# Kernel tuning notes

Hardware: AMD Instinct MI355X
Metric: run time of the kernel (lower is better)

Reference implementation:

```python
import jax, jax.numpy as jnp
import numpy as np

# Scalars from init_kwargs (qat_training=False inference path)
IN_ZP = 0
OUT_ZP = 0
IN_SCALE = 0.02
OUT_SCALE = 0.05
STRIDE = (1, 1)
PAD = (1, 1)      # (ph, pw); module pads (pw, pw, ph, ph) via F.pad
DIL = (1, 1)
GROUPS = 1
QMIN, QMAX = -128, 127  # get_quantized_range(8)


def setup_inputs() -> dict:
    key = jax.random.key(0)
    k1, k2, k3, k4 = jax.random.split(key, 4)
    x = jax.random.randint(k1, (32, 128, 56, 56), -128, 128, dtype=jnp.int32).astype(jnp.int8)
    weight = jax.random.randint(k2, (256, 128, 3, 3), -128, 128, dtype=jnp.int32).astype(jnp.int8)
    bias = jax.random.randint(k3, (256,), -1000, 1000, dtype=jnp.int32)
    weight_scale = jax.random.uniform(k4, (256,), minval=1e-3, maxval=1e-2, dtype=jnp.float32)
    return {"x": x, "weight": weight, "bias": bias, "weight_scale": weight_scale}


def reference(x, weight, bias, weight_scale):
    # Pad spatial dims with the input zero point (matches F.pad(..., value=input_zero_point))
    xp = jnp.pad(x.astype(jnp.int32),
                 ((0, 0), (0, 0), (PAD[0], PAD[0]), (PAD[1], PAD[1])),
                 constant_values=IN_ZP)
    # Exact int32-accumulate convolution (torch CPU path)
    acc = jax.lax.conv_general_dilated(
        xp, weight.astype(jnp.int32),
        window_strides=STRIDE, padding='VALID', rhs_dilation=DIL,
        dimension_numbers=('NCHW', 'OIHW', 'NCHW'),
        feature_group_count=GROUPS, preferred_element_type=jnp.int32)
    acc = acc + bias[None, :, None, None]
    # Per-output-channel requantization
    scale = (IN_SCALE * weight_scale / OUT_SCALE)[None, :, None, None]
    out = acc.astype(jnp.float32) * scale + OUT_ZP
    out = jnp.clip(jnp.round(out), QMIN, QMAX).astype(jnp.int8)
    return out
```

## Files before the change

kernel.cpp:

```cpp
#include <hip/hip_runtime.h>
#include <hip/hip_bf16.h>
#include <stdint.h>


#define NB   32
#define CIN  128
#define HO   56
#define WO   56
#define KOUT 256
#define HP   58
#define ROWB (HP * CIN)

typedef int v4i  __attribute__((ext_vector_type(4)));
typedef int v16i __attribute__((ext_vector_type(16)));

static __device__ __forceinline__ void gload_lds16(const int8_t* g, int8_t* l) {
  __builtin_amdgcn_global_load_lds(
      (const __attribute__((address_space(1))) void*)g,
      (__attribute__((address_space(3))) void*)l, 16, 0, 0);
}

__global__ __launch_bounds__(256) void pack_x_kernel(const int* __restrict__ x,
                                                     int8_t* __restrict__ xp) {
  __shared__ int t32[128][57];
  const int tid = threadIdx.x;
  const int r = blockIdx.x;
  const int n = blockIdx.y;
  const bool interior = (r >= 1) && (r <= HO);

  if (interior) {
    const int h = r - 1;
    const int* xrow = x + ((size_t)(n * CIN) * HO + h) * WO;
    #pragma unroll
    for (int it = 0; it < 7; ++it) {
      const int j = it * 256 + tid;
      const int c = j / 14;
      const int w4 = j - c * 14;
      const int4 v = *reinterpret_cast<const int4*>(xrow + c * 3136 + w4 * 4);
      t32[c][w4 * 4 + 0] = v.x;
      t32[c][w4 * 4 + 1] = v.y;
      t32[c][w4 * 4 + 2] = v.z;
      t32[c][w4 * 4 + 3] = v.w;
    }
  }
  __syncthreads();
  #pragma unroll
  for (int it = 0; it < 8; ++it) {
    const int i = it * 256 + tid;
    if (i < HP * 32) {
      const int w = i >> 5;
      const int c4 = i & 31;
      int vv = 0;
      if (interior && w >= 1 && w <= WO) {
        const int b0 = t32[c4 * 4 + 0][w - 1] & 0xff;
        const int b1 = t32[c4 * 4 + 1][w - 1] & 0xff;
        const int b2 = t32[c4 * 4 + 2][w - 1] & 0xff;
        const int b3 = t32[c4 * 4 + 3][w - 1];
        vv = b0 | (b1 << 8) | (b2 << 16) | (b3 << 24);
      }
      *reinterpret_cast<int*>(xp + ((size_t)(n * HP + r) * HP + w) * CIN + c4 * 4) = vv;
    }
  }
}

__global__ __launch_bounds__(256) void pack_w_kernel(const int* __restrict__ wgt,
                                                     int8_t* __restrict__ wq) {
  const int wid = blockIdx.x * 256 + threadIdx.x;
  const int wi = wid & 3;
  const int ci = wid >> 2;
  const int ktb = ci / 9216;
  const int r  = ci - ktb * 9216;
  const int tap = r >> 10;
  const int r2  = r & 1023;
  const int cc  = r2 >> 7;
  const int ch  = r2 & 127;
  const int k_global = ktb * 128 + ch;
  const int cin0 = cc * 16 + wi * 4;
  const int base = (k_global * CIN + cin0) * 9 + tap;
  const int v0 = wgt[base];
  const int v1 = wgt[base + 9];
  const int v2 = wgt[base + 18];
  const int v3 = wgt[base + 27];
  reinterpret_cast<int*>(wq)[wid] =
      (v0 & 0xff) | ((v1 & 0xff) << 8) | ((v2 & 0xff) << 16) | (v3 << 24);
}

__global__ __launch_bounds__(256, 2) void conv_kernel(const int8_t* __restrict__ xp,
                                                      const int8_t* __restrict__ wq,
                                                      const int* __restrict__ bias,
                                                      const float* __restrict__ wscale,
                                                      int* __restrict__ out) {
  __shared__ __align__(16) int8_t lw[2][8 * 128 * 16];
  __shared__ __align__(16) int8_t lx[6 * HP * 8 * 16];
  __shared__ int   bsh[128];
  __shared__ float ssh[128];

  const int tid = threadIdx.x;
  const int rg = blockIdx.x;
  const int n_img = blockIdx.y;
  const int ktb = blockIdx.z;
  const int h0 = rg * 4;

  const int lane = tid & 63;
  const int wr = tid >> 6;
  const int p0 = lane & 31;
  const int half = lane >> 5;

  const int8_t* xg = xp + ((size_t)(n_img * HP) + h0) * ROWB;
  const int8_t* wqt = wq + (size_t)ktb * (9 * 16384);

  #pragma unroll
  for (int it = 0; it < 11; ++it) {
    const int i = it * 256 + tid;
    if (i < 6 * HP * 8) {
      const int pf = i >> 3;
      const int cc = (i & 7) ^ (pf & 7);
      gload_lds16(xg + pf * CIN + (cc << 4), lx + i * 16);
    }
  }
  #pragma unroll
  for (int it = 0; it < 4; ++it) {
    const int j = it * 256 + tid;
    gload_lds16(wqt + j * 16, lw[0] + j * 16);
  }
  if (tid < 128) {
    const int ch = ktb * 128 + tid;
    bsh[tid] = bias[ch];
    ssh[tid] = (0.02f * wscale[ch]) / 0.05f;
  }
  __syncthreads();

  v16i acc[4][2];
  #pragma unroll
  for (int mt = 0; mt < 4; ++mt)
    #pragma unroll
    for (int nt = 0; nt < 2; ++nt)
      #pragma unroll
      for (int e = 0; e < 16; ++e) acc[mt][nt][e] = 0;

  #pragma unroll
  for (int tap = 0; tap < 9; ++tap) {
    if (tap < 8) {
      const int8_t* wsrc = wqt + (tap + 1) * 16384;
      int8_t* ldst = lw[(tap + 1) & 1];
      #pragma unroll
      for (int it = 0; it < 4; ++it) {
        const int j = it * 256 + tid;
        gload_lds16(wsrc + j * 16, ldst + j * 16);
      }
    }
    const int kh = tap / 3, kw = tap - kh * 3;
    const int8_t* lwt = lw[tap & 1];
    const int pfb = (wr + kh) * HP + kw;
    #pragma unroll
    for (int ks = 0; ks < 4; ++ks) {
      const int cch = 2 * ks + half;
      v4i a[4];
      #pragma unroll
      for (int mt = 0; mt < 4; ++mt)
        a[mt] = *reinterpret_cast<const v4i*>(lwt + cch * 2048 + (mt * 32 + p0) * 16);
      #pragma unroll
      for (int nt = 0; nt < 2; ++nt) {
        const int pf = pfb + nt * 32 + p0;
        const v4i b = *reinterpret_cast<const v4i*>(
            lx + pf * CIN + ((cch ^ (pf & 7)) << 4));
        #pragma unroll
        for (int mt = 0; mt < 4; ++mt)
          acc[mt][nt] = __builtin_amdgcn_mfma_i32_32x32x32_i8(a[mt], b, acc[mt][nt], 0, 0, 0);
      }
    }
    __syncthreads();
  }

  const int h = h0 + wr;
  #pragma unroll
  for (int mt = 0; mt < 4; ++mt) {
    #pragma unroll
    for (int r = 0; r < 16; ++r) {
      const int cl = mt * 32 + (r & 3) + 8 * (r >> 2) + 4 * half;
      const int bi = bsh[cl];
      const float sc = ssh[cl];
      int* ob = out + (((size_t)(n_img * KOUT + ktb * 128 + cl)) * HO + h) * WO;
      #pragma unroll
      for (int nt = 0; nt < 2; ++nt) {
        const int w = nt * 32 + p0;
        if (w < WO) {
          float v = (float)(acc[mt][nt][r] + bi) * sc;
          v = rintf(v);
          v = fminf(fmaxf(v, -128.0f), 127.0f);
          ob[w] = (int)v;
        }
      }
    }
  }
}

extern "C" void kernel_launch(void* const* d_in, const int* in_sizes, int n_in,
                              void* d_out, int out_size, void* d_ws, size_t ws_size,
                              hipStream_t stream) {
  const int* x = (const int*)d_in[0];
  const int* wgt = (const int*)d_in[1];
  const int* bias = (const int*)d_in[2];
  const float* wscale = (const float*)d_in[3];
  int* out = (int*)d_out;

  int8_t* xp = (int8_t*)d_ws;
  int8_t* wq = (int8_t*)d_ws + (size_t)NB * HP * ROWB;

  pack_x_kernel<<<dim3(HP, NB), 256, 0, stream>>>(x, xp);
  pack_w_kernel<<<288, 256, 0, stream>>>(wgt, wq);
  conv_kernel<<<dim3(14, 32, 2), 256, 0, stream>>>(xp, wq, bias, wscale, out);
}
```

Measured before the change: 182.5 us.

## Split conv block across 8 waves, halving per-wave output channels

The conv kernel now runs 512 threads per block. Each of the 8 waves computes 64 output channels instead of 128, so the accumulator register footprint per wave is halved and more waves can be resident. The LDS x buffer gets padding rows, because wave rows can read slightly past the loaded region. s_setprio is placed around the MFMA group to favour issuing matrix ops. Each wave now loads B fragments that duplicate those of its partner wave, which adds LDS read traffic per MFMA.

Measured after the change: 182.9 us. Within noise of the previous version (+0.2%).

```diff
diff --git a/kernel.cpp b/kernel.cpp
--- a/kernel.cpp
+++ b/kernel.cpp
@@ -85,13 +85,13 @@
       (v0 & 0xff) | ((v1 & 0xff) << 8) | ((v2 & 0xff) << 16) | (v3 << 24);
 }
 
-__global__ __launch_bounds__(256, 2) void conv_kernel(const int8_t* __restrict__ xp,
+__global__ __launch_bounds__(512, 4) void conv_kernel(const int8_t* __restrict__ xp,
                                                       const int8_t* __restrict__ wq,
                                                       const int* __restrict__ bias,
                                                       const float* __restrict__ wscale,
                                                       int* __restrict__ out) {
   __shared__ __align__(16) int8_t lw[2][8 * 128 * 16];
-  __shared__ __align__(16) int8_t lx[6 * HP * 8 * 16];
+  __shared__ __align__(16) int8_t lx[(6 * HP + 8) * 8 * 16];
   __shared__ int   bsh[128];
   __shared__ float ssh[128];
 
@@ -102,7 +102,9 @@
   const int h0 = rg * 4;
 
   const int lane = tid & 63;
-  const int wr = tid >> 6;
+  const int wid = tid >> 6;
+  const int wr = wid & 3;
+  const int wh = wid >> 2;
   const int p0 = lane & 31;
   const int half = lane >> 5;
 
@@ -110,19 +112,16 @@
   const int8_t* wqt = wq + (size_t)ktb * (9 * 16384);
 
   #pragma unroll
-  for (int it = 0; it < 11; ++it) {
-    const int i = it * 256 + tid;
+  for (int it = 0; it < 6; ++it) {
+    const int i = it * 512 + tid;
     if (i < 6 * HP * 8) {
       const int pf = i >> 3;
       const int cc = (i & 7) ^ (pf & 7);
       gload_lds16(xg + pf * CIN + (cc << 4), lx + i * 16);
     }
   }
-  #pragma unroll
-  for (int it = 0; it < 4; ++it) {
-    const int j = it * 256 + tid;
-    gload_lds16(wqt + j * 16, lw[0] + j * 16);
-  }
+  gload_lds16(wqt + tid * 16, lw[0] + tid * 16);
+  gload_lds16(wqt + (512 + tid) * 16, lw[0] + (512 + tid) * 16);
   if (tid < 128) {
     const int ch = ktb * 128 + tid;
     bsh[tid] = bias[ch];
@@ -130,54 +129,53 @@
   }
   __syncthreads();
 
-  v16i acc[4][2];
-  #pragma unroll
-  for (int mt = 0; mt < 4; ++mt)
+  v16i acc[2][2];
+  #pragma unroll
+  for (int mt = 0; mt < 2; ++mt)
     #pragma unroll
     for (int nt = 0; nt < 2; ++nt)
       #pragma unroll
       for (int e = 0; e < 16; ++e) acc[mt][nt][e] = 0;
+
+  const int chb = wh * 64;
 
   #pragma unroll
   for (int tap = 0; tap < 9; ++tap) {
     if (tap < 8) {
       const int8_t* wsrc = wqt + (tap + 1) * 16384;
       int8_t* ldst = lw[(tap + 1) & 1];
-      #pragma unroll
-      for (int it = 0; it < 4; ++it) {
-        const int j = it * 256 + tid;
-        gload_lds16(wsrc + j * 16, ldst + j * 16);
-      }
-    }
-    const int kh = tap / 3, kw = tap - kh * 3;
+      gload_lds16(wsrc + tid * 16, ldst + tid * 16);
+      gload_lds16(wsrc + (512 + tid) * 16, ldst + (512 + tid) * 16);
+    }
+    const int kh = (tap >= 3) + (tap >= 6);
+    const int kw = tap - 3 * kh;
     const int8_t* lwt = lw[tap & 1];
     const int pfb = (wr + kh) * HP + kw;
     #pragma unroll
     for (int ks = 0; ks < 4; ++ks) {
       const int cch = 2 * ks + half;
-      v4i a[4];
-      #pragma unroll
-      for (int mt = 0; mt < 4; ++mt)
-        a[mt] = *reinterpret_cast<const v4i*>(lwt + cch * 2048 + (mt * 32 + p0) * 16);
-      #pragma unroll
-      for (int nt = 0; nt < 2; ++nt) {
-        const int pf = pfb + nt * 32 + p0;
-        const v4i b = *reinterpret_cast<const v4i*>(
-            lx + pf * CIN + ((cch ^ (pf & 7)) << 4));
-        #pragma unroll
-        for (int mt = 0; mt < 4; ++mt)
-          acc[mt][nt] = __builtin_amdgcn_mfma_i32_32x32x32_i8(a[mt], b, acc[mt][nt], 0, 0, 0);
-      }
+      const v4i a0 = *reinterpret_cast<const v4i*>(lwt + cch * 2048 + (chb + p0) * 16);
+      const v4i a1 = *reinterpret_cast<const v4i*>(lwt + cch * 2048 + (chb + 32 + p0) * 16);
+      const int pf0 = pfb + p0;
+      const int pf1 = pfb + 32 + p0;
+      const v4i b0 = *reinterpret_cast<const v4i*>(lx + pf0 * CIN + ((cch ^ (pf0 & 7)) << 4));
+      const v4i b1 = *reinterpret_cast<const v4i*>(lx + pf1 * CIN + ((cch ^ (pf1 & 7)) << 4));
+      __builtin_amdgcn_s_setprio(1);
+      acc[0][0] = __builtin_amdgcn_mfma_i32_32x32x32_i8(a0, b0, acc[0][0], 0, 0, 0);
+      acc[1][0] = __builtin_amdgcn_mfma_i32_32x32x32_i8(a1, b0, acc[1][0], 0, 0, 0);
+      acc[0][1] = __builtin_amdgcn_mfma_i32_32x32x32_i8(a0, b1, acc[0][1], 0, 0, 0);
+      acc[1][1] = __builtin_amdgcn_mfma_i32_32x32x32_i8(a1, b1, acc[1][1], 0, 0, 0);
+      __builtin_amdgcn_s_setprio(0);
     }
     __syncthreads();
   }
 
   const int h = h0 + wr;
   #pragma unroll
-  for (int mt = 0; mt < 4; ++mt) {
+  for (int mt = 0; mt < 2; ++mt) {
     #pragma unroll
     for (int r = 0; r < 16; ++r) {
-      const int cl = mt * 32 + (r & 3) + 8 * (r >> 2) + 4 * half;
+      const int cl = chb + mt * 32 + (r & 3) + 8 * (r >> 2) + 4 * half;
       const int bi = bsh[cl];
       const float sc = ssh[cl];
       int* ob = out + (((size_t)(n_img * KOUT + ktb * 128 + cl)) * HO + h) * WO;
@@ -209,5 +207,5 @@
 
   pack_x_kernel<<<dim3(HP, NB), 256, 0, stream>>>(x, xp);
   pack_w_kernel<<<288, 256, 0, stream>>>(wgt, wq);
-  conv_kernel<<<dim3(14, 32, 2), 256, 0, stream>>>(xp, wq, bias, wscale, out);
-}
+  conv_kernel<<<dim3(14, 32, 2), 512, 0, stream>>>(xp, wq, bias, wscale, out);
+}
```

## Halve conv block to two waves each computing two output rows

Applied to the files above, without the earlier changes.

Each conv block now runs two wavefronts instead of four, and each wave computes two output rows, so every A fragment loaded from LDS feeds sixteen MFMAs instead of eight. The aim is to cut LDS read traffic per MFMA and raise register-level reuse of the weight fragments. The MFMA burst is wrapped in s_setprio to favour matrix issue. In exchange, accumulator registers double to 256 VGPRs per lane and there are fewer waves to hide load latency. The x tile buffer also gets extra padding, presumably to cover reads past the tile edge for the last rows.

After: 190.0 us. 1.04x slower.

```diff
diff --git a/kernel.cpp b/kernel.cpp
--- a/kernel.cpp
+++ b/kernel.cpp
@@ -85,13 +85,13 @@
       (v0 & 0xff) | ((v1 & 0xff) << 8) | ((v2 & 0xff) << 16) | (v3 << 24);
 }
 
-__global__ __launch_bounds__(256, 2) void conv_kernel(const int8_t* __restrict__ xp,
+__global__ __launch_bounds__(128, 1) void conv_kernel(const int8_t* __restrict__ xp,
                                                       const int8_t* __restrict__ wq,
                                                       const int* __restrict__ bias,
                                                       const float* __restrict__ wscale,
                                                       int* __restrict__ out) {
   __shared__ __align__(16) int8_t lw[2][8 * 128 * 16];
-  __shared__ __align__(16) int8_t lx[6 * HP * 8 * 16];
+  __shared__ __align__(16) int8_t lx[(6 * HP + 8) * 8 * 16];
   __shared__ int   bsh[128];
   __shared__ float ssh[128];
 
@@ -110,8 +110,8 @@
   const int8_t* wqt = wq + (size_t)ktb * (9 * 16384);
 
   #pragma unroll
-  for (int it = 0; it < 11; ++it) {
-    const int i = it * 256 + tid;
+  for (int it = 0; it < 22; ++it) {
+    const int i = it * 128 + tid;
     if (i < 6 * HP * 8) {
       const int pf = i >> 3;
       const int cc = (i & 7) ^ (pf & 7);
@@ -119,24 +119,23 @@
     }
   }
   #pragma unroll
-  for (int it = 0; it < 4; ++it) {
-    const int j = it * 256 + tid;
+  for (int k = 0; k < 8; ++k) {
+    const int j = k * 128 + tid;
     gload_lds16(wqt + j * 16, lw[0] + j * 16);
   }
-  if (tid < 128) {
-    const int ch = ktb * 128 + tid;
-    bsh[tid] = bias[ch];
-    ssh[tid] = (0.02f * wscale[ch]) / 0.05f;
-  }
+  bsh[tid] = bias[ktb * 128 + tid];
+  ssh[tid] = (0.02f * wscale[ktb * 128 + tid]) / 0.05f;
   __syncthreads();
 
-  v16i acc[4][2];
+  v16i acc[4][2][2];
   #pragma unroll
   for (int mt = 0; mt < 4; ++mt)
     #pragma unroll
-    for (int nt = 0; nt < 2; ++nt)
-      #pragma unroll
-      for (int e = 0; e < 16; ++e) acc[mt][nt][e] = 0;
+    for (int lr = 0; lr < 2; ++lr)
+      #pragma unroll
+      for (int nt = 0; nt < 2; ++nt)
+        #pragma unroll
+        for (int e = 0; e < 16; ++e) acc[mt][lr][nt][e] = 0;
 
   #pragma unroll
   for (int tap = 0; tap < 9; ++tap) {
@@ -144,35 +143,44 @@
       const int8_t* wsrc = wqt + (tap + 1) * 16384;
       int8_t* ldst = lw[(tap + 1) & 1];
       #pragma unroll
-      for (int it = 0; it < 4; ++it) {
-        const int j = it * 256 + tid;
+      for (int k = 0; k < 8; ++k) {
+        const int j = k * 128 + tid;
         gload_lds16(wsrc + j * 16, ldst + j * 16);
       }
     }
-    const int kh = tap / 3, kw = tap - kh * 3;
+    const int kh = (tap >= 3) + (tap >= 6);
+    const int kw = tap - 3 * kh;
     const int8_t* lwt = lw[tap & 1];
-    const int pfb = (wr + kh) * HP + kw;
     #pragma unroll
     for (int ks = 0; ks < 4; ++ks) {
       const int cch = 2 * ks + half;
-      v4i a[4];
+      v4i a[4], b[2][2];
       #pragma unroll
       for (int mt = 0; mt < 4; ++mt)
         a[mt] = *reinterpret_cast<const v4i*>(lwt + cch * 2048 + (mt * 32 + p0) * 16);
       #pragma unroll
-      for (int nt = 0; nt < 2; ++nt) {
-        const int pf = pfb + nt * 32 + p0;
-        const v4i b = *reinterpret_cast<const v4i*>(
-            lx + pf * CIN + ((cch ^ (pf & 7)) << 4));
-        #pragma unroll
-        for (int mt = 0; mt < 4; ++mt)
-          acc[mt][nt] = __builtin_amdgcn_mfma_i32_32x32x32_i8(a[mt], b, acc[mt][nt], 0, 0, 0);
-      }
+      for (int lr = 0; lr < 2; ++lr) {
+        const int pfb = (wr * 2 + lr + kh) * HP + kw;
+        #pragma unroll
+        for (int nt = 0; nt < 2; ++nt) {
+          const int pf = pfb + nt * 32 + p0;
+          b[lr][nt] = *reinterpret_cast<const v4i*>(lx + pf * CIN + ((cch ^ (pf & 7)) << 4));
+        }
+      }
+      __builtin_amdgcn_s_setprio(1);
+      #pragma unroll
+      for (int mt = 0; mt < 4; ++mt)
+        #pragma unroll
+        for (int lr = 0; lr < 2; ++lr)
+          #pragma unroll
+          for (int nt = 0; nt < 2; ++nt)
+            acc[mt][lr][nt] = __builtin_amdgcn_mfma_i32_32x32x32_i8(
+                a[mt], b[lr][nt], acc[mt][lr][nt], 0, 0, 0);
+      __builtin_amdgcn_s_setprio(0);
     }
     __syncthreads();
   }
 
-  const int h = h0 + wr;
   #pragma unroll
   for (int mt = 0; mt < 4; ++mt) {
     #pragma unroll
@@ -180,15 +188,19 @@
       const int cl = mt * 32 + (r & 3) + 8 * (r >> 2) + 4 * half;
       const int bi = bsh[cl];
       const float sc = ssh[cl];
-      int* ob = out + (((size_t)(n_img * KOUT + ktb * 128 + cl)) * HO + h) * WO;
-      #pragma unroll
-      for (int nt = 0; nt < 2; ++nt) {
-        const int w = nt * 32 + p0;
-        if (w < WO) {
-          float v = (float)(acc[mt][nt][r] + bi) * sc;
-          v = rintf(v);
-          v = fminf(fmaxf(v, -128.0f), 127.0f);
-          ob[w] = (int)v;
+      #pragma unroll
+      for (int lr = 0; lr < 2; ++lr) {
+        const int h = h0 + wr * 2 + lr;
+        int* ob = out + (((size_t)(n_img * KOUT + ktb * 128 + cl)) * HO + h) * WO;
+        #pragma unroll
+        for (int nt = 0; nt < 2; ++nt) {
+          const int w = nt * 32 + p0;
+          if (w < WO) {
+            float v = (float)(acc[mt][lr][nt][r] + bi) * sc;
+            v = rintf(v);
+            v = fminf(fmaxf(v, -128.0f), 127.0f);
+            ob[w] = (int)v;
+          }
         }
       }
     }
@@ -209,5 +221,5 @@
 
   pack_x_kernel<<<dim3(HP, NB), 256, 0, stream>>>(x, xp);
   pack_w_kernel<<<288, 256, 0, stream>>>(wgt, wq);
-  conv_kernel<<<dim3(14, 32, 2), 256, 0, stream>>>(xp, wq, bias, wscale, out);
-}
+  conv_kernel<<<dim3(14, 32, 2), 128, 0, stream>>>(xp, wq, bias, wscale, out);
+}
```

## Use 512-thread blocks covering 8 output rows with new LDS swizzle

Applied to the files above, without the earlier changes.

Doubles the conv block to 512 threads (8 waves), each block now producing 8 output rows, so each weight tap loaded to LDS feeds twice as many rows and halo input rows are a smaller share of the loaded tile. The input LDS tile now pairs pixels into 256-byte groups with an XOR swizzle on the pair index, which changes the bank-conflict pattern of the B-operand reads. MFMA issue is wrapped in s_setprio and the B loads are hoisted. LDS use grows to about 107KB per block and the grid shrinks to 448 blocks, so occupancy and wave count per CU change.

After: 183.4 us. Within noise of the previous version (+0.5%).

```diff
diff --git a/kernel.cpp b/kernel.cpp
--- a/kernel.cpp
+++ b/kernel.cpp
@@ -85,13 +85,13 @@
       (v0 & 0xff) | ((v1 & 0xff) << 8) | ((v2 & 0xff) << 16) | (v3 << 24);
 }
 
-__global__ __launch_bounds__(256, 2) void conv_kernel(const int8_t* __restrict__ xp,
+__global__ __launch_bounds__(512, 2) void conv_kernel(const int8_t* __restrict__ xp,
                                                       const int8_t* __restrict__ wq,
                                                       const int* __restrict__ bias,
                                                       const float* __restrict__ wscale,
                                                       int* __restrict__ out) {
   __shared__ __align__(16) int8_t lw[2][8 * 128 * 16];
-  __shared__ __align__(16) int8_t lx[6 * HP * 8 * 16];
+  __shared__ __align__(16) int8_t lx[4704 * 16];
   __shared__ int   bsh[128];
   __shared__ float ssh[128];
 
@@ -99,7 +99,7 @@
   const int rg = blockIdx.x;
   const int n_img = blockIdx.y;
   const int ktb = blockIdx.z;
-  const int h0 = rg * 4;
+  const int h0 = rg * 8;
 
   const int lane = tid & 63;
   const int wr = tid >> 6;
@@ -110,19 +110,18 @@
   const int8_t* wqt = wq + (size_t)ktb * (9 * 16384);
 
   #pragma unroll
-  for (int it = 0; it < 11; ++it) {
-    const int i = it * 256 + tid;
-    if (i < 6 * HP * 8) {
-      const int pf = i >> 3;
-      const int cc = (i & 7) ^ (pf & 7);
+  for (int it = 0; it < 10; ++it) {
+    const int i = it * 512 + tid;
+    if (i < 4640) {
+      const int qf = i >> 4;
+      const int s = i & 15;
+      const int pf = qf * 2 + (s >> 3);
+      const int cc = (s & 7) ^ (qf & 7);
       gload_lds16(xg + pf * CIN + (cc << 4), lx + i * 16);
     }
   }
-  #pragma unroll
-  for (int it = 0; it < 4; ++it) {
-    const int j = it * 256 + tid;
-    gload_lds16(wqt + j * 16, lw[0] + j * 16);
-  }
+  gload_lds16(wqt + tid * 16,         lw[0] + tid * 16);
+  gload_lds16(wqt + (512 + tid) * 16, lw[0] + (512 + tid) * 16);
   if (tid < 128) {
     const int ch = ktb * 128 + tid;
     bsh[tid] = bias[ch];
@@ -143,15 +142,18 @@
     if (tap < 8) {
       const int8_t* wsrc = wqt + (tap + 1) * 16384;
       int8_t* ldst = lw[(tap + 1) & 1];
-      #pragma unroll
-      for (int it = 0; it < 4; ++it) {
-        const int j = it * 256 + tid;
-        gload_lds16(wsrc + j * 16, ldst + j * 16);
-      }
-    }
-    const int kh = tap / 3, kw = tap - kh * 3;
+      gload_lds16(wsrc + tid * 16,         ldst + tid * 16);
+      gload_lds16(wsrc + (512 + tid) * 16, ldst + (512 + tid) * 16);
+    }
+    const int kh = (tap >= 3) + (tap >= 6);
+    const int kw = tap - 3 * kh;
     const int8_t* lwt = lw[tap & 1];
-    const int pfb = (wr + kh) * HP + kw;
+    const int pf0 = (wr + kh) * HP + kw + p0;
+    const int pf1 = pf0 + 32;
+    const int8_t* bbase0 = lx + ((pf0 >> 1) << 8) + ((pf0 & 1) << 7);
+    const int8_t* bbase1 = lx + ((pf1 >> 1) << 8) + ((pf1 & 1) << 7);
+    const int q70 = (pf0 >> 1) & 7;
+    const int q71 = (pf1 >> 1) & 7;
     #pragma unroll
     for (int ks = 0; ks < 4; ++ks) {
       const int cch = 2 * ks + half;
@@ -159,15 +161,15 @@
       #pragma unroll
       for (int mt = 0; mt < 4; ++mt)
         a[mt] = *reinterpret_cast<const v4i*>(lwt + cch * 2048 + (mt * 32 + p0) * 16);
-      #pragma unroll
-      for (int nt = 0; nt < 2; ++nt) {
-        const int pf = pfb + nt * 32 + p0;
-        const v4i b = *reinterpret_cast<const v4i*>(
-            lx + pf * CIN + ((cch ^ (pf & 7)) << 4));
-        #pragma unroll
-        for (int mt = 0; mt < 4; ++mt)
-          acc[mt][nt] = __builtin_amdgcn_mfma_i32_32x32x32_i8(a[mt], b, acc[mt][nt], 0, 0, 0);
+      const v4i b0 = *reinterpret_cast<const v4i*>(bbase0 + ((cch ^ q70) << 4));
+      const v4i b1 = *reinterpret_cast<const v4i*>(bbase1 + ((cch ^ q71) << 4));
+      __builtin_amdgcn_s_setprio(1);
+      #pragma unroll
+      for (int mt = 0; mt < 4; ++mt) {
+        acc[mt][0] = __builtin_amdgcn_mfma_i32_32x32x32_i8(a[mt], b0, acc[mt][0], 0, 0, 0);
+        acc[mt][1] = __builtin_amdgcn_mfma_i32_32x32x32_i8(a[mt], b1, acc[mt][1], 0, 0, 0);
       }
+      __builtin_amdgcn_s_setprio(0);
     }
     __syncthreads();
   }
@@ -209,5 +211,5 @@
 
   pack_x_kernel<<<dim3(HP, NB), 256, 0, stream>>>(x, xp);
   pack_w_kernel<<<288, 256, 0, stream>>>(wgt, wq);
-  conv_kernel<<<dim3(14, 32, 2), 256, 0, stream>>>(xp, wq, bias, wscale, out);
-}
+  conv_kernel<<<dim3(7, 32, 2), 512, 0, stream>>>(xp, wq, bias, wscale, out);
+}
```
